# Kernel optimization log

Hardware: AMD Instinct MI355X
Metric: run time of the kernel (lower is better)

Reference implementation:

```python
import jax, jax.numpy as jnp
import numpy as np

SIGMA = 1.0      # diffusion scale (gamma_t = sigma * ones)
ALPHA = 1.0      # OU mean-reversion rate
DIM = 128        # state dimension
HIDDEN = 512     # drift-MLP hidden width
DT = 0.05
NSTEPS = 20      # tfinal/dt with uniform_step_scheme -> 21 ts, 20 steps
BATCH = 16384


def _drift(y, t, W1, b1, W2, b2):
    """Drift network u_t(y, t): 2-layer tanh MLP on concat(y, t)."""
    t_col = jnp.full((y.shape[0], 1), t, dtype=y.dtype)
    h = jnp.tanh(jnp.concatenate([y, t_col], axis=-1) @ W1 + b1)
    return h @ W2 + b2  # [B, DIM]


def setup_inputs() -> dict:
    key = jax.random.key(0)
    k0, k1, k2, k3 = jax.random.split(key, 4)
    # init_sample: y0 ~ N(0, sigma^2) (stationary OU prior)
    y0 = SIGMA * jax.random.normal(k0, (BATCH, DIM), dtype=jnp.float32)
    W1 = 0.05 * jax.random.normal(k1, (DIM + 1, HIDDEN), dtype=jnp.float32)
    b1 = jnp.zeros((HIDDEN,), jnp.float32)
    W2 = 0.05 * jax.random.normal(k2, (HIDDEN, DIM), dtype=jnp.float32)
    b2 = jnp.zeros((DIM,), jnp.float32)
    # pre-drawn standard normal Brownian increments (scaled by sqrt(dt) in step)
    noises = jax.random.normal(k3, (NSTEPS, BATCH, DIM), dtype=jnp.float32)
    # uniform_step_scheme(0, tfinal, dt)
    ts = jnp.arange(NSTEPS + 1, dtype=jnp.float32) * DT
    return {"y0": y0, "W1": W1, "b1": b1, "W2": W2, "b2": b2,
            "noises": noises, "ts": ts}


def reference(y0, W1, b1, W2, b2, noises, ts):
    """Euler-Maruyama integration of the augmented OU Foellmer SDE (STL).

    Augmented state [B, DIM+3]: [y, int u/sigma . dW, int sg(u)/sigma . dW,
    int |u|^2/(2 sigma^2) dt] matching f_aug/g_aug/g_prod of the module.
    """
    B = y0.shape[0]
    y_aug0 = jnp.concatenate([y0, jnp.zeros((B, 3), y0.dtype)], axis=-1)

    def step(carry, inp):
        y_aug, t_pas = carry
        t, noise = inp
        dt = t - t_pas
        sq = jnp.sqrt(dt)
        y = y_aug[:, :DIM]
        u = _drift(y, t_pas, W1, b1, W2, b2)          # f_aug[..., :dim]
        u_det = jax.lax.stop_gradient(u)              # detached_drift (STL)
        # y-part: OU prior drift -alpha*y + control u, diffusion sigma dW
        y_new = y + (u - ALPHA * y) * dt + SIGMA * sq * noise
        # augmented channels (g_prod einsum 'ij,ij->i' terms and energy)
        udw = jnp.einsum('bd,bd->b', u, noise) * (sq / SIGMA)
        udw_det = jnp.einsum('bd,bd->b', u_det, noise) * (sq / SIGMA)
        energy = 0.5 * jnp.sum(u * u, axis=-1) / (SIGMA ** 2) * dt
        aug = y_aug[:, DIM:] + jnp.stack([udw, udw_det, energy], axis=-1)
        y_aug_new = jnp.concatenate([y_new, aug], axis=-1)
        return (y_aug_new, t), y_aug_new

    (_, _), traj_tail = jax.lax.scan(step, (y_aug0, ts[0]), (ts[1:], noises))
    param_trajectory = jnp.concatenate([y_aug0[None], traj_tail], axis=0)  # [T+1, B, DIM+3]
    return param_trajectory, ts
```

## Files before the change

### kernel.cpp

```cpp
#include <hip/hip_runtime.h>
#include <math.h>

#define DIM 128
#define HID 512
#define BATCHN 16384
#define NSTEPS 20
#define ROWSTRIDE 131
#define SLICE (BATCHN * ROWSTRIDE)
#define BM 32
#define HCST 520
#define YBST 136
#define REDST 18

typedef __bf16 bf16_t;
typedef __bf16 bf16x8 __attribute__((ext_vector_type(8)));
typedef float floatx4 __attribute__((ext_vector_type(4)));

__device__ __forceinline__ float fast_tanh(float x) {
    float e = __expf(2.0f * x);
    return 1.0f - 2.0f / (e + 1.0f);
}

__global__ void prep_kernel(const float* __restrict__ W1, const float* __restrict__ b1,
                            const float* __restrict__ W2, const float* __restrict__ ts,
                            bf16_t* __restrict__ W1T, bf16_t* __restrict__ W2T,
                            float* __restrict__ biasEff) {
    int tid = blockIdx.x * blockDim.x + threadIdx.x;
    {   int j = tid >> 7, k = tid & 127;
        W1T[j * DIM + k] = (bf16_t)W1[k * HID + j]; }
    {   int j = tid >> 9, k = tid & 511;
        W2T[j * HID + k] = (bf16_t)W2[k * DIM + j]; }
    if (tid < NSTEPS * HID) {
        int s = tid >> 9, j = tid & 511;
        biasEff[tid] = b1[j] + ts[s] * W1[DIM * HID + j];
    }
}

__global__ __launch_bounds__(512, 2)
void fused_kernel(const float* __restrict__ y0, float* __restrict__ traj,
                  const float* __restrict__ noises,
                  const bf16_t* __restrict__ W1T, const bf16_t* __restrict__ W2T,
                  const float* __restrict__ biasEff, const float* __restrict__ b2,
                  const float* __restrict__ ts) {
    __shared__ __align__(16) char smem[61056];
    bf16_t* ybf    = (bf16_t*)smem;
    bf16_t* hc     = (bf16_t*)(smem + 8704);
    float*  outImg = (float*)(smem + 41984);
    float*  red    = (float*)(smem + 58752);

    const int tid  = threadIdx.x;
    const int lane = tid & 63;
    const int w    = tid >> 6;
    const int quad = lane >> 4;
    const int l15  = lane & 15;
    const int row0 = blockIdx.x * BM;
    const int col  = w * 16 + l15;

    bf16x8 w1f[4][4];
    {
        const bf16_t* W1w = W1T + (size_t)(w * 64) * DIM;
        #pragma unroll
        for (int jn = 0; jn < 4; ++jn)
            #pragma unroll
            for (int k0 = 0; k0 < 4; ++k0)
                w1f[jn][k0] = *(const bf16x8*)(W1w + (jn * 16 + l15) * DIM + k0 * 32 + quad * 8);
    }
    bf16x8 w2f[16];
    {
        const bf16_t* W2r = W2T + (size_t)col * HID + quad * 8;
        #pragma unroll
        for (int k0 = 0; k0 < 16; ++k0)
            w2f[k0] = *(const bf16x8*)(W2r + k0 * 32);
    }
    const float b2c = b2[col];

    float yv[2][4];
    {
        const float* y0b = y0 + (size_t)row0 * DIM;
        #pragma unroll
        for (int m = 0; m < 2; ++m)
            #pragma unroll
            for (int i = 0; i < 4; ++i) {
                int r = m * 16 + quad * 4 + i;
                float v = y0b[(size_t)r * DIM + col];
                yv[m][i] = v;
                outImg[r * ROWSTRIDE + col] = v;
                ybf[r * YBST + col] = (bf16_t)v;
            }
    }
    float aug0 = 0.f, aug2 = 0.f;
    if (tid < BM) {
        float* o = outImg + tid * ROWSTRIDE + DIM;
        o[0] = 0.f; o[1] = 0.f; o[2] = 0.f;
    }
    if (blockIdx.x == 0 && tid <= NSTEPS)
        traj[(size_t)(NSTEPS + 1) * SLICE + tid] = ts[tid];
    __syncthreads();
    {
        float* dst = traj + (size_t)row0 * ROWSTRIDE;
        const floatx4* srcv = (const floatx4*)outImg;
        for (int i2 = tid; i2 < (BM * ROWSTRIDE) / 4; i2 += 512)
            ((floatx4*)dst)[i2] = srcv[i2];
    }

    #pragma unroll 1
    for (int s = 0; s < NSTEPS; ++s) {
        const float dt = ts[s + 1] - ts[s];
        const float sq = sqrtf(dt);

        float nz[2][4];
        {
            const float* nb = noises + (size_t)s * (BATCHN * DIM) + (size_t)row0 * DIM;
            #pragma unroll
            for (int m = 0; m < 2; ++m)
                #pragma unroll
                for (int i = 0; i < 4; ++i)
                    nz[m][i] = nb[(size_t)(m * 16 + quad * 4 + i) * DIM + col];
        }
        float bias[4];
        {
            const float* be = biasEff + s * HID + w * 64;
            #pragma unroll
            for (int jn = 0; jn < 4; ++jn) bias[jn] = be[jn * 16 + l15];
        }

        bf16x8 a1[2][4];
        #pragma unroll
        for (int m = 0; m < 2; ++m)
            #pragma unroll
            for (int k0 = 0; k0 < 4; ++k0)
                a1[m][k0] = *(const bf16x8*)(ybf + (m * 16 + l15) * YBST + k0 * 32 + quad * 8);

        #pragma unroll
        for (int jn = 0; jn < 4; ++jn) {
            floatx4 acc1[2];
            acc1[0] = (floatx4){0.f, 0.f, 0.f, 0.f};
            acc1[1] = (floatx4){0.f, 0.f, 0.f, 0.f};
            #pragma unroll
            for (int k0 = 0; k0 < 4; ++k0) {
                acc1[0] = __builtin_amdgcn_mfma_f32_16x16x32_bf16(a1[0][k0], w1f[jn][k0], acc1[0], 0, 0, 0);
                acc1[1] = __builtin_amdgcn_mfma_f32_16x16x32_bf16(a1[1][k0], w1f[jn][k0], acc1[1], 0, 0, 0);
            }
            #pragma unroll
            for (int m = 0; m < 2; ++m)
                #pragma unroll
                for (int i = 0; i < 4; ++i)
                    hc[(m * 16 + quad * 4 + i) * HCST + w * 64 + jn * 16 + l15] =
                        (bf16_t)fast_tanh(acc1[m][i] + bias[jn]);
        }
        __syncthreads();

        floatx4 accu[2];
        accu[0] = (floatx4){0.f, 0.f, 0.f, 0.f};
        accu[1] = (floatx4){0.f, 0.f, 0.f, 0.f};
        #pragma unroll
        for (int k0 = 0; k0 < 16; ++k0) {
            bf16x8 a20 = *(const bf16x8*)(hc + l15 * HCST + k0 * 32 + quad * 8);
            bf16x8 a21 = *(const bf16x8*)(hc + (16 + l15) * HCST + k0 * 32 + quad * 8);
            accu[0] = __builtin_amdgcn_mfma_f32_16x16x32_bf16(a20, w2f[k0], accu[0], 0, 0, 0);
            accu[1] = __builtin_amdgcn_mfma_f32_16x16x32_bf16(a21, w2f[k0], accu[1], 0, 0, 0);
        }

        #pragma unroll
        for (int m = 0; m < 2; ++m)
            #pragma unroll
            for (int i = 0; i < 4; ++i) {
                int r = m * 16 + quad * 4 + i;
                float u  = accu[m][i] + b2c;
                float y  = yv[m][i];
                float yn = y + (u - y) * dt + sq * nz[m][i];
                yv[m][i] = yn;
                outImg[r * ROWSTRIDE + col] = yn;
                ybf[r * YBST + col] = (bf16_t)yn;
                float pdu = u * nz[m][i];
                float pen = u * u;
                pdu += __shfl_xor(pdu, 1); pen += __shfl_xor(pen, 1);
                pdu += __shfl_xor(pdu, 2); pen += __shfl_xor(pen, 2);
                pdu += __shfl_xor(pdu, 4); pen += __shfl_xor(pen, 4);
                pdu += __shfl_xor(pdu, 8); pen += __shfl_xor(pen, 8);
                if (l15 == 0) {
                    red[r * REDST + w * 2]     = pdu;
                    red[r * REDST + w * 2 + 1] = pen;
                }
            }
        __syncthreads();

        if (tid < BM) {
            const float* rp = red + tid * REDST;
            float du = 0.f, en = 0.f;
            #pragma unroll
            for (int k = 0; k < 8; ++k) { du += rp[k * 2]; en += rp[k * 2 + 1]; }
            aug0 += du * sq;
            aug2 += 0.5f * en * dt;
            float* o = outImg + tid * ROWSTRIDE + DIM;
            o[0] = aug0; o[1] = aug0; o[2] = aug2;
        }
        __syncthreads();

        {
            float* dst = traj + (size_t)(s + 1) * SLICE + (size_t)row0 * ROWSTRIDE;
            const floatx4* srcv = (const floatx4*)outImg;
            for (int i2 = tid; i2 < (BM * ROWSTRIDE) / 4; i2 += 512)
                ((floatx4*)dst)[i2] = srcv[i2];
        }
    }
}

extern "C" void kernel_launch(void* const* d_in, const int* in_sizes, int n_in,
                              void* d_out, int out_size, void* d_ws, size_t ws_size,
                              hipStream_t stream) {
    const float* y0     = (const float*)d_in[0];
    const float* W1     = (const float*)d_in[1];
    const float* b1     = (const float*)d_in[2];
    const float* W2     = (const float*)d_in[3];
    const float* b2     = (const float*)d_in[4];
    const float* noises = (const float*)d_in[5];
    const float* ts     = (const float*)d_in[6];
    float* out = (float*)d_out;

    bf16_t* W1T     = (bf16_t*)d_ws;
    bf16_t* W2T     = (bf16_t*)((char*)d_ws + 131072);
    float*  biasEff = (float*)((char*)d_ws + 262144);

    prep_kernel<<<256, 256, 0, stream>>>(W1, b1, W2, ts, W1T, W2T, biasEff);
    fused_kernel<<<BATCHN / BM, 512, 0, stream>>>(y0, out, noises, W1T, W2T,
                                                  biasEff, b2, ts);
}
```

Before: 490.6 us.

## Interleave two row groups per block in a software-pipelined step schedule

Each block now handles 64 rows split into two 32-row groups whose GEMM1, GEMM2/epilogue, reduction-combine and trajectory store phases are staggered. This cuts the per-step barriers from three to one per phase and overlaps MFMA work of one group with the other's epilogue and global stores. It also adds XOR swizzling of the bf16 LDS tiles to reduce bank conflicts, and precomputes dt/sqrt tables in shared memory. LDS use rises to about 156 KB, which likely limits occupancy to one block per CU despite launch_bounds(512,2), and the grid is halved to 256 blocks.

```diff
diff --git a/kernel.cpp b/kernel.cpp
--- a/kernel.cpp
+++ b/kernel.cpp
@@ -7,7 +7,8 @@
 #define NSTEPS 20
 #define ROWSTRIDE 131
 #define SLICE (BATCHN * ROWSTRIDE)
-#define BM 32
+#define BM 64
+#define GR 32
 #define HCST 520
 #define YBST 136
 #define REDST 18
@@ -36,17 +37,140 @@
     }
 }
 
+
+__device__ __forceinline__ void do_gemm1(
+    int s, const bf16_t* __restrict__ ybfX, bf16_t* __restrict__ hcX,
+    float (&nz)[2][4], const bf16x8 (&w1f)[4][4],
+    const float* __restrict__ noises, int gRow0,
+    const float* __restrict__ biasEff,
+    int quad, int l15, int w, int col)
+{
+    const float* nb = noises + (size_t)s * (BATCHN * DIM) + (size_t)gRow0 * DIM;
+    #pragma unroll
+    for (int m = 0; m < 2; ++m)
+        #pragma unroll
+        for (int i = 0; i < 4; ++i)
+            nz[m][i] = nb[(size_t)(m * 16 + quad * 4 + i) * DIM + col];
+    float bias[4];
+    const float* be = biasEff + s * HID + w * 64;
+    #pragma unroll
+    for (int jn = 0; jn < 4; ++jn) bias[jn] = be[jn * 16 + l15];
+
+    const int rsw = (l15 >> 3) << 4;
+    bf16x8 a1[2][4];
+    #pragma unroll
+    for (int m = 0; m < 2; ++m)
+        #pragma unroll
+        for (int k0 = 0; k0 < 4; ++k0)
+            a1[m][k0] = *(const bf16x8*)(ybfX + (m * 16 + l15) * YBST +
+                                         ((k0 * 32 + quad * 8) ^ rsw));
+    const int wsw = (quad >> 1) << 4;
+    #pragma unroll
+    for (int jn = 0; jn < 4; ++jn) {
+        floatx4 acc1[2];
+        acc1[0] = (floatx4){0.f, 0.f, 0.f, 0.f};
+        acc1[1] = (floatx4){0.f, 0.f, 0.f, 0.f};
+        #pragma unroll
+        for (int k0 = 0; k0 < 4; ++k0) {
+            acc1[0] = __builtin_amdgcn_mfma_f32_16x16x32_bf16(a1[0][k0], w1f[jn][k0], acc1[0], 0, 0, 0);
+            acc1[1] = __builtin_amdgcn_mfma_f32_16x16x32_bf16(a1[1][k0], w1f[jn][k0], acc1[1], 0, 0, 0);
+        }
+        #pragma unroll
+        for (int m = 0; m < 2; ++m)
+            #pragma unroll
+            for (int i = 0; i < 4; ++i)
+                hcX[(m * 16 + quad * 4 + i) * HCST + ((w * 64 + jn * 16 + l15) ^ wsw)] =
+                    (bf16_t)fast_tanh(acc1[m][i] + bias[jn]);
+    }
+}
+
+__device__ __forceinline__ void do_gemm2_epi(
+    const bf16_t* __restrict__ hcY, bf16_t* __restrict__ ybfY,
+    float* __restrict__ outY, float* __restrict__ redY,
+    float (&yv)[2][4], const float (&nz)[2][4],
+    const bf16x8 (&w2f)[16], float b2c, float dtv, float sqv,
+    int quad, int l15, int w, int col)
+{
+    const int rsw = (l15 >> 3) << 4;
+    floatx4 accu[2];
+    accu[0] = (floatx4){0.f, 0.f, 0.f, 0.f};
+    accu[1] = (floatx4){0.f, 0.f, 0.f, 0.f};
+    #pragma unroll
+    for (int k0 = 0; k0 < 16; ++k0) {
+        bf16x8 a20 = *(const bf16x8*)(hcY + l15 * HCST + ((k0 * 32 + quad * 8) ^ rsw));
+        bf16x8 a21 = *(const bf16x8*)(hcY + (16 + l15) * HCST + ((k0 * 32 + quad * 8) ^ rsw));
+        accu[0] = __builtin_amdgcn_mfma_f32_16x16x32_bf16(a20, w2f[k0], accu[0], 0, 0, 0);
+        accu[1] = __builtin_amdgcn_mfma_f32_16x16x32_bf16(a21, w2f[k0], accu[1], 0, 0, 0);
+    }
+    const int wsw = (quad >> 1) << 4;
+    #pragma unroll
+    for (int m = 0; m < 2; ++m)
+        #pragma unroll
+        for (int i = 0; i < 4; ++i) {
+            int r = m * 16 + quad * 4 + i;
+            float u  = accu[m][i] + b2c;
+            float y  = yv[m][i];
+            float yn = y + (u - y) * dtv + sqv * nz[m][i];
+            yv[m][i] = yn;
+            outY[r * ROWSTRIDE + col] = yn;
+            ybfY[r * YBST + (col ^ wsw)] = (bf16_t)yn;
+            float pdu = u * nz[m][i];
+            float pen = u * u;
+            pdu += __shfl_xor(pdu, 1); pen += __shfl_xor(pen, 1);
+            pdu += __shfl_xor(pdu, 2); pen += __shfl_xor(pen, 2);
+            pdu += __shfl_xor(pdu, 4); pen += __shfl_xor(pen, 4);
+            pdu += __shfl_xor(pdu, 8); pen += __shfl_xor(pen, 8);
+            if (l15 == 0) {
+                redY[r * REDST + w * 2]     = pdu;
+                redY[r * REDST + w * 2 + 1] = pen;
+            }
+        }
+}
+
+__device__ __forceinline__ void do_comb(
+    const float* __restrict__ redX, float* __restrict__ outX,
+    float& a0, float& a2v, bool act, int r, float dtv, float sqv)
+{
+    if (act) {
+        const float* rp = redX + r * REDST;
+        float du = 0.f, en = 0.f;
+        #pragma unroll
+        for (int k = 0; k < 8; ++k) { du += rp[k * 2]; en += rp[k * 2 + 1]; }
+        a0  += du * sqv;
+        a2v += 0.5f * en * dtv;
+        float* o = outX + r * ROWSTRIDE + DIM;
+        o[0] = a0; o[1] = a0; o[2] = a2v;
+    }
+}
+
+__device__ __forceinline__ void do_stream(
+    const float* __restrict__ src, float* __restrict__ dst, int tid)
+{
+    const floatx4* s4 = (const floatx4*)src;
+    floatx4* d4 = (floatx4*)dst;
+    for (int i = tid; i < GR * ROWSTRIDE / 4; i += 512)
+        d4[i] = s4[i];
+}
+
 __global__ __launch_bounds__(512, 2)
 void fused_kernel(const float* __restrict__ y0, float* __restrict__ traj,
                   const float* __restrict__ noises,
                   const bf16_t* __restrict__ W1T, const bf16_t* __restrict__ W2T,
                   const float* __restrict__ biasEff, const float* __restrict__ b2,
                   const float* __restrict__ ts) {
-    __shared__ __align__(16) char smem[61056];
-    bf16_t* ybf    = (bf16_t*)smem;
-    bf16_t* hc     = (bf16_t*)(smem + 8704);
-    float*  outImg = (float*)(smem + 41984);
-    float*  red    = (float*)(smem + 58752);
+    __shared__ __align__(16) char smem[155808];
+    bf16_t* ybfA = (bf16_t*)(smem);
+    bf16_t* ybfB = (bf16_t*)(smem + 8704);
+    bf16_t* hcA  = (bf16_t*)(smem + 17408);
+    bf16_t* hcB  = (bf16_t*)(smem + 50688);
+    float*  outA0 = (float*)(smem + 83968);
+    float*  outA1 = (float*)(smem + 100736);
+    float*  outB0 = (float*)(smem + 117504);
+    float*  outB1 = (float*)(smem + 134272);
+    float*  redA = (float*)(smem + 151040);
+    float*  redB = (float*)(smem + 153344);
+    float*  dtbl = (float*)(smem + 155648);
+    float*  sqtbl = (float*)(smem + 155728);
 
     const int tid  = threadIdx.x;
     const int lane = tid & 63;
@@ -74,135 +198,92 @@
     }
     const float b2c = b2[col];
 
-    float yv[2][4];
+    float yvA[2][4], yvB[2][4], nzA[2][4], nzB[2][4];
+    float augA0 = 0.f, augA2 = 0.f, augB0 = 0.f, augB2 = 0.f;
     {
+        const int wsw = (quad >> 1) << 4;
         const float* y0b = y0 + (size_t)row0 * DIM;
         #pragma unroll
         for (int m = 0; m < 2; ++m)
             #pragma unroll
             for (int i = 0; i < 4; ++i) {
                 int r = m * 16 + quad * 4 + i;
-                float v = y0b[(size_t)r * DIM + col];
-                yv[m][i] = v;
-                outImg[r * ROWSTRIDE + col] = v;
-                ybf[r * YBST + col] = (bf16_t)v;
+                float va = y0b[(size_t)r * DIM + col];
+                float vb = y0b[(size_t)(r + GR) * DIM + col];
+                yvA[m][i] = va;  yvB[m][i] = vb;
+                outA0[r * ROWSTRIDE + col] = va;
+                outB0[r * ROWSTRIDE + col] = vb;
+                ybfA[r * YBST + (col ^ wsw)] = (bf16_t)va;
+                ybfB[r * YBST + (col ^ wsw)] = (bf16_t)vb;
             }
-    }
-    float aug0 = 0.f, aug2 = 0.f;
-    if (tid < BM) {
-        float* o = outImg + tid * ROWSTRIDE + DIM;
-        o[0] = 0.f; o[1] = 0.f; o[2] = 0.f;
-    }
-    if (blockIdx.x == 0 && tid <= NSTEPS)
-        traj[(size_t)(NSTEPS + 1) * SLICE + tid] = ts[tid];
+        if (tid < GR) {
+            float* oa = outA0 + tid * ROWSTRIDE + DIM;
+            oa[0] = 0.f; oa[1] = 0.f; oa[2] = 0.f;
+        } else if (tid < 2 * GR) {
+            float* ob = outB0 + (tid - GR) * ROWSTRIDE + DIM;
+            ob[0] = 0.f; ob[1] = 0.f; ob[2] = 0.f;
+        }
+        if (tid < NSTEPS) {
+            float d = ts[tid + 1] - ts[tid];
+            dtbl[tid] = d;
+            sqtbl[tid] = sqrtf(d);
+        }
+        if (blockIdx.x == 0 && tid <= NSTEPS)
+            traj[(size_t)(NSTEPS + 1) * SLICE + tid] = ts[tid];
+    }
     __syncthreads();
-    {
-        float* dst = traj + (size_t)row0 * ROWSTRIDE;
-        const floatx4* srcv = (const floatx4*)outImg;
-        for (int i2 = tid; i2 < (BM * ROWSTRIDE) / 4; i2 += 512)
-            ((floatx4*)dst)[i2] = srcv[i2];
-    }
+    do_stream(outA0, traj + (size_t)row0 * ROWSTRIDE, tid);
+    do_stream(outB0, traj + (size_t)(row0 + GR) * ROWSTRIDE, tid);
 
     #pragma unroll 1
-    for (int s = 0; s < NSTEPS; ++s) {
-        const float dt = ts[s + 1] - ts[s];
-        const float sq = sqrtf(dt);
-
-        float nz[2][4];
-        {
-            const float* nb = noises + (size_t)s * (BATCHN * DIM) + (size_t)row0 * DIM;
-            #pragma unroll
-            for (int m = 0; m < 2; ++m)
-                #pragma unroll
-                for (int i = 0; i < 4; ++i)
-                    nz[m][i] = nb[(size_t)(m * 16 + quad * 4 + i) * DIM + col];
-        }
-        float bias[4];
-        {
-            const float* be = biasEff + s * HID + w * 64;
-            #pragma unroll
-            for (int jn = 0; jn < 4; ++jn) bias[jn] = be[jn * 16 + l15];
-        }
-
-        bf16x8 a1[2][4];
-        #pragma unroll
-        for (int m = 0; m < 2; ++m)
-            #pragma unroll
-            for (int k0 = 0; k0 < 4; ++k0)
-                a1[m][k0] = *(const bf16x8*)(ybf + (m * 16 + l15) * YBST + k0 * 32 + quad * 8);
-
-        #pragma unroll
-        for (int jn = 0; jn < 4; ++jn) {
-            floatx4 acc1[2];
-            acc1[0] = (floatx4){0.f, 0.f, 0.f, 0.f};
-            acc1[1] = (floatx4){0.f, 0.f, 0.f, 0.f};
-            #pragma unroll
-            for (int k0 = 0; k0 < 4; ++k0) {
-                acc1[0] = __builtin_amdgcn_mfma_f32_16x16x32_bf16(a1[0][k0], w1f[jn][k0], acc1[0], 0, 0, 0);
-                acc1[1] = __builtin_amdgcn_mfma_f32_16x16x32_bf16(a1[1][k0], w1f[jn][k0], acc1[1], 0, 0, 0);
+    for (int p = 0; p <= 2 * NSTEPS + 2; ++p) {
+        const int h = p >> 1;
+        if ((p & 1) == 0) {
+            const int sg1 = h, sg2 = h - 1, sc = h - 1, ss = h - 2;
+            const bool g1 = (sg1 < NSTEPS);
+            const bool g2 = (sg2 >= 0) && (sg2 < NSTEPS);
+            const bool gc = (sc >= 0) && (sc < NSTEPS);
+            const bool gs = (ss >= 0) && (ss < NSTEPS);
+            float* outE = (sg2 >= 0 && (sg2 & 1)) ? outB1 : outB0;
+            float* outC = (sc >= 0 && (sc & 1)) ? outA1 : outA0;
+            const float* outS = (ss >= 0 && (ss & 1)) ? outB1 : outB0;
+            float dtE = g2 ? dtbl[sg2] : 0.f, sqE = g2 ? sqtbl[sg2] : 0.f;
+            float dtC = gc ? dtbl[sc] : 0.f, sqC = gc ? sqtbl[sc] : 0.f;
+            if (g1 && g2 && gc && gs) {
+                do_gemm1(sg1, ybfA, hcA, nzA, w1f, noises, row0, biasEff, quad, l15, w, col);
+                do_gemm2_epi(hcB, ybfB, outE, redB, yvB, nzB, w2f, b2c, dtE, sqE, quad, l15, w, col);
+                do_comb(redA, outC, augA0, augA2, tid < GR, tid, dtC, sqC);
+                do_stream(outS, traj + (size_t)(ss + 1) * SLICE + (size_t)(row0 + GR) * ROWSTRIDE, tid);
+            } else {
+                if (g1) do_gemm1(sg1, ybfA, hcA, nzA, w1f, noises, row0, biasEff, quad, l15, w, col);
+                if (g2) do_gemm2_epi(hcB, ybfB, outE, redB, yvB, nzB, w2f, b2c, dtE, sqE, quad, l15, w, col);
+                if (gc) do_comb(redA, outC, augA0, augA2, tid < GR, tid, dtC, sqC);
+                if (gs) do_stream(outS, traj + (size_t)(ss + 1) * SLICE + (size_t)(row0 + GR) * ROWSTRIDE, tid);
             }
-            #pragma unroll
-            for (int m = 0; m < 2; ++m)
-                #pragma unroll
-                for (int i = 0; i < 4; ++i)
-                    hc[(m * 16 + quad * 4 + i) * HCST + w * 64 + jn * 16 + l15] =
-                        (bf16_t)fast_tanh(acc1[m][i] + bias[jn]);
+        } else {
+            const int sg1 = h, sg2 = h, sc = h - 1, ss = h - 1;
+            const bool g1 = (sg1 < NSTEPS);
+            const bool g2 = (sg2 < NSTEPS);
+            const bool gc = (sc >= 0) && (sc < NSTEPS);
+            const bool gs = (ss >= 0) && (ss < NSTEPS);
+            float* outE = (sg2 & 1) ? outA1 : outA0;
+            float* outC = (sc >= 0 && (sc & 1)) ? outB1 : outB0;
+            const float* outS = (ss >= 0 && (ss & 1)) ? outA1 : outA0;
+            float dtE = g2 ? dtbl[sg2] : 0.f, sqE = g2 ? sqtbl[sg2] : 0.f;
+            float dtC = gc ? dtbl[sc] : 0.f, sqC = gc ? sqtbl[sc] : 0.f;
+            if (g1 && g2 && gc && gs) {
+                do_gemm1(sg1, ybfB, hcB, nzB, w1f, noises, row0 + GR, biasEff, quad, l15, w, col);
+                do_gemm2_epi(hcA, ybfA, outE, redA, yvA, nzA, w2f, b2c, dtE, sqE, quad, l15, w, col);
+                do_comb(redB, outC, augB0, augB2, (tid >= GR) && (tid < 2 * GR), tid & (GR - 1), dtC, sqC);
+                do_stream(outS, traj + (size_t)(ss + 1) * SLICE + (size_t)row0 * ROWSTRIDE, tid);
+            } else {
+                if (g1) do_gemm1(sg1, ybfB, hcB, nzB, w1f, noises, row0 + GR, biasEff, quad, l15, w, col);
+                if (g2) do_gemm2_epi(hcA, ybfA, outE, redA, yvA, nzA, w2f, b2c, dtE, sqE, quad, l15, w, col);
+                if (gc) do_comb(redB, outC, augB0, augB2, (tid >= GR) && (tid < 2 * GR), tid & (GR - 1), dtC, sqC);
+                if (gs) do_stream(outS, traj + (size_t)(ss + 1) * SLICE + (size_t)row0 * ROWSTRIDE, tid);
+            }
         }
         __syncthreads();
-
-        floatx4 accu[2];
-        accu[0] = (floatx4){0.f, 0.f, 0.f, 0.f};
-        accu[1] = (floatx4){0.f, 0.f, 0.f, 0.f};
-        #pragma unroll
-        for (int k0 = 0; k0 < 16; ++k0) {
-            bf16x8 a20 = *(const bf16x8*)(hc + l15 * HCST + k0 * 32 + quad * 8);
-            bf16x8 a21 = *(const bf16x8*)(hc + (16 + l15) * HCST + k0 * 32 + quad * 8);
-            accu[0] = __builtin_amdgcn_mfma_f32_16x16x32_bf16(a20, w2f[k0], accu[0], 0, 0, 0);
-            accu[1] = __builtin_amdgcn_mfma_f32_16x16x32_bf16(a21, w2f[k0], accu[1], 0, 0, 0);
-        }
-
-        #pragma unroll
-        for (int m = 0; m < 2; ++m)
-            #pragma unroll
-            for (int i = 0; i < 4; ++i) {
-                int r = m * 16 + quad * 4 + i;
-                float u  = accu[m][i] + b2c;
-                float y  = yv[m][i];
-                float yn = y + (u - y) * dt + sq * nz[m][i];
-                yv[m][i] = yn;
-                outImg[r * ROWSTRIDE + col] = yn;
-                ybf[r * YBST + col] = (bf16_t)yn;
-                float pdu = u * nz[m][i];
-                float pen = u * u;
-                pdu += __shfl_xor(pdu, 1); pen += __shfl_xor(pen, 1);
-                pdu += __shfl_xor(pdu, 2); pen += __shfl_xor(pen, 2);
-                pdu += __shfl_xor(pdu, 4); pen += __shfl_xor(pen, 4);
-                pdu += __shfl_xor(pdu, 8); pen += __shfl_xor(pen, 8);
-                if (l15 == 0) {
-                    red[r * REDST + w * 2]     = pdu;
-                    red[r * REDST + w * 2 + 1] = pen;
-                }
-            }
-        __syncthreads();
-
-        if (tid < BM) {
-            const float* rp = red + tid * REDST;
-            float du = 0.f, en = 0.f;
-            #pragma unroll
-            for (int k = 0; k < 8; ++k) { du += rp[k * 2]; en += rp[k * 2 + 1]; }
-            aug0 += du * sq;
-            aug2 += 0.5f * en * dt;
-            float* o = outImg + tid * ROWSTRIDE + DIM;
-            o[0] = aug0; o[1] = aug0; o[2] = aug2;
-        }
-        __syncthreads();
-
-        {
-            float* dst = traj + (size_t)(s + 1) * SLICE + (size_t)row0 * ROWSTRIDE;
-            const floatx4* srcv = (const floatx4*)outImg;
-            for (int i2 = tid; i2 < (BM * ROWSTRIDE) / 4; i2 += 512)
-                ((floatx4*)dst)[i2] = srcv[i2];
-        }
     }
 }
 
```

New measurement: 964.0 us. 1.96x slower.
